# Kernel optimization log

Hardware: AMD Instinct MI355X
Metric: run time of the kernel (lower is better)

Reference implementation:

```python
import jax, jax.numpy as jnp
from jax import lax
import numpy as np

BOHR = 0.52917721067  # Angstrom per Bohr (au.BOHR)
DAMP_MUTUAL = 0.39
DAMP_FIELD = 0.7
N_ITER = 7  # fixed-point iterations for induced dipoles


def setup_inputs() -> dict:
    key = jax.random.key(0)
    N = 100000
    deg = 32
    E = N * deg
    k1, k2, k3, k4, k5, k6, k7 = jax.random.split(key, 7)
    edge_src = jax.random.randint(k1, (E,), 0, N)
    edge_dst = jax.random.randint(k2, (E,), 0, N)
    # realistic interatomic distances in [1, 6] Angstrom (avoid r ~ 0)
    distances = 1.0 + 5.0 * jax.random.uniform(k3, (E,), dtype=jnp.float32)
    u = jax.random.normal(k4, (E, 3), dtype=jnp.float32)
    u = u / jnp.linalg.norm(u, axis=-1, keepdims=True)
    vec = u * distances[:, None]  # consistent |vec| == distances
    polarisability = 0.5 + 1.5 * jax.random.uniform(k5, (N,), dtype=jnp.float32)
    charges = 0.3 * jax.random.normal(k6, (N,), dtype=jnp.float32)
    species = jax.random.randint(k7, (N,), 1, 10)
    return {
        "species": species,
        "edge_src": edge_src,
        "edge_dst": edge_dst,
        "distances": distances,
        "vec": vec,
        "polarisability": polarisability,
        "charges": charges,
    }


def reference(species, edge_src, edge_dst, distances, vec, polarisability, charges):
    N = polarisability.shape[0]
    # convert to atomic units
    rij = distances / BOHR                      # [E]
    vec_ij = vec / BOHR                         # [E,3]
    pol = polarisability.reshape(-1) / BOHR**3  # [N]

    # Thole damping: u_ij^3 = r^3 / sqrt(alpha_i * alpha_j)
    alpha_ij = pol[edge_src] * pol[edge_dst]
    uij3 = rij**3 / jnp.sqrt(alpha_ij)
    exp_m = jnp.exp(-DAMP_MUTUAL * uij3)
    l3_m = 1.0 - exp_m
    l5_m = 1.0 - (1.0 + DAMP_MUTUAL * uij3) * exp_m
    l3_f = 1.0 - jnp.exp(-DAMP_FIELD * uij3)

    inv_r3 = 1.0 / rij**3
    inv_r5 = inv_r3 / rij**2

    # permanent (charge) electric field at src atoms, Thole-damped
    e_edges = (l3_f * charges[edge_dst] * inv_r3)[:, None] * vec_ij  # [E,3]
    E0 = jax.ops.segment_sum(e_edges, edge_src, num_segments=N)      # [N,3]

    alpha = pol[:, None]  # isotropic polarisability [N,1]

    def matvec(mu):
        # Thole-damped dipole-dipole interaction tensor applied to mu: (T mu)_i
        mu_d = mu[edge_dst]                                   # [E,3]
        dot = jnp.sum(vec_ij * mu_d, axis=-1)                 # [E]
        t = (l3_m * inv_r3)[:, None] * mu_d \
            - (3.0 * l5_m * inv_r5 * dot)[:, None] * vec_ij   # [E,3]
        return jax.ops.segment_sum(t, edge_src, num_segments=N)

    # iterative induced dipoles: mu = alpha * (E0 - T mu)
    mu0 = alpha * E0

    def step(mu, _):
        return alpha * (E0 - matvec(mu)), None

    mu, _ = lax.scan(step, mu0, None, length=N_ITER)

    # per-atom polarisation energy: -1/2 mu . E0
    energy = -0.5 * jnp.sum(mu * E0, axis=-1)  # [N]
    return energy
```

## Files before the change

### kernel.cpp

```cpp
#include <hip/hip_runtime.h>
#include <hip/hip_fp16.h>


static constexpr float INV_B  = 1.0f / 0.52917721067f;
static constexpr float INV_B3 = INV_B * INV_B * INV_B;
static constexpr float DM = 0.39f;
static constexpr float DF = 0.7f;
static constexpr int   NITER = 7;
#define SCAN_B 1024
#define STAGE 4096
#define BUILD_T 512
#define MAXBUCK 512

__device__ inline unsigned packh2(float a, float b) {
    return (unsigned)__half_as_ushort(__float2half_rn(a)) |
           ((unsigned)__half_as_ushort(__float2half_rn(b)) << 16);
}
__device__ inline float unph_lo(unsigned u) {
    return __half2float(__ushort_as_half((unsigned short)(u & 0xFFFFu)));
}
__device__ inline float unph_hi(unsigned u) {
    return __half2float(__ushort_as_half((unsigned short)(u >> 16)));
}


__global__ void bhist_kernel(const int* __restrict__ esrc, int* __restrict__ h,
                             int E, int nbuck, int nblk, int chunk)
{
    __shared__ int cnt[MAXBUCK];
    int tid = threadIdx.x, blk = blockIdx.x;
    for (int b = tid; b < nbuck; b += blockDim.x) cnt[b] = 0;
    __syncthreads();
    int lo = blk * chunk, hi = min(E, lo + chunk);
    for (int i = lo + tid; i < hi; i += blockDim.x)
        atomicAdd(&cnt[esrc[i] >> 8], 1);
    __syncthreads();
    for (int b = tid; b < nbuck; b += blockDim.x)
        h[b * nblk + blk] = cnt[b];
}


__global__ void scan1_kernel(const int* __restrict__ in, int* __restrict__ excl,
                             int* __restrict__ blocksum, int n)
{
    __shared__ int sh[SCAN_B];
    int tid = threadIdx.x;
    int i = blockIdx.x * SCAN_B + tid;
    int v = (i < n) ? in[i] : 0;
    sh[tid] = v;
    __syncthreads();
    for (int off = 1; off < SCAN_B; off <<= 1) {
        int t = (tid >= off) ? sh[tid - off] : 0;
        __syncthreads();
        sh[tid] += t;
        __syncthreads();
    }
    if (i < n) excl[i] = sh[tid] - v;
    if (tid == SCAN_B - 1) blocksum[blockIdx.x] = sh[tid];
}

__global__ void scan2_kernel(int* __restrict__ blocksum, int nb)
{
    __shared__ int sh[1024];
    int tid = threadIdx.x;
    int v = (tid < nb) ? blocksum[tid] : 0;
    sh[tid] = v;
    __syncthreads();
    for (int off = 1; off < 1024; off <<= 1) {
        int t = (tid >= off) ? sh[tid - off] : 0;
        __syncthreads();
        sh[tid] += t;
        __syncthreads();
    }
    if (tid < nb) blocksum[tid] = sh[tid] - v;
}

__global__ void scan3_kernel(int* __restrict__ excl, const int* __restrict__ blocksum, int n)
{
    int i = blockIdx.x * SCAN_B + threadIdx.x;
    if (i < n) excl[i] += blocksum[blockIdx.x];
}


__global__ void bktptr_kernel(const int* __restrict__ hoff,
                              int* __restrict__ bktptr, int* __restrict__ rowptr,
                              int nbuck, int nblk, int N, int E)
{
    int b = blockIdx.x * blockDim.x + threadIdx.x;
    if (b < nbuck) bktptr[b] = hoff[b * nblk];
    if (b == nbuck) {
        bktptr[b] = E;
        if (rowptr) rowptr[N] = E;
    }
}


__global__ __launch_bounds__(BUILD_T)
void build_kernel(const int* __restrict__ esrc, const int* __restrict__ edst,
                  const float* __restrict__ dist, const float* __restrict__ vec,
                  const float* __restrict__ pol, const float* __restrict__ chg,
                  const int* __restrict__ hoff,
                  uint4* __restrict__ recs, int E, int nbuck, int nblk, int chunk)
{
    __shared__ uint4 stg[STAGE];
    __shared__ unsigned short sbuck[STAGE];
    __shared__ int wcur[MAXBUCK];
    __shared__ int shist[MAXBUCK];
    __shared__ int sbase[MAXBUCK];
    __shared__ int scur[MAXBUCK];
    __shared__ int wsum[8];
    int tid = threadIdx.x, blk = blockIdx.x;
    int lane = tid & 63, wav = tid >> 6;
    int lo = blk * chunk, hi = min(E, lo + chunk), cnt = hi - lo;

    if (tid < nbuck) wcur[tid] = hoff[tid * nblk + blk];
    __syncthreads();

    int nsb = (cnt + STAGE - 1) / STAGE;
    for (int sb = 0; sb < nsb; ++sb) {
        int s0 = sb * STAGE, s1 = min(cnt, s0 + STAGE), scnt = s1 - s0;
        if (tid < nbuck) shist[tid] = 0;
        __syncthreads();
        for (int i = s0 + tid; i < s1; i += BUILD_T)
            atomicAdd(&shist[esrc[lo + i] >> 8], 1);
        __syncthreads();
        int v = (tid < nbuck) ? shist[tid] : 0;
        int x = v;
        #pragma unroll
        for (int off = 1; off < 64; off <<= 1) {
            int t = __shfl_up(x, off);
            if (lane >= off) x += t;
        }
        if (lane == 63) wsum[wav] = x;
        __syncthreads();
        if (tid < 8) {
            int w = wsum[tid];
            #pragma unroll
            for (int off = 1; off < 8; off <<= 1) {
                int t = __shfl_up(w, off, 8);
                if (tid >= off) w += t;
            }
            wsum[tid] = w;
        }
        __syncthreads();
        int base = (wav > 0) ? wsum[wav - 1] : 0;
        if (tid < nbuck) {
            int ex = x + base - v;
            sbase[tid] = ex;
            scur[tid]  = ex;
        }
        __syncthreads();
        for (int i = s0 + tid; i < s1; i += BUILD_T) {
            int gi = lo + i;
            int s = esrc[gi], d = edst[gi];
            int b = s >> 8;
            float r  = dist[gi] * INV_B;
            float vx = vec[3*gi+0] * INV_B;
            float vy = vec[3*gi+1] * INV_B;
            float vz = vec[3*gi+2] * INV_B;
            float ps = pol[s] * INV_B3;
            float pd = pol[d] * INV_B3;
            float r2 = r * r;
            float r3 = r2 * r;
            float u  = r3 * rsqrtf(ps * pd);
            float em = __expf(-DM * u);
            float l3m = 1.0f - em;
            float l5m = 1.0f - (1.0f + DM * u) * em;
            float inv_r3 = 1.0f / r3;
            float inv_r5 = inv_r3 / r2;
            float c1 = l3m * inv_r3;
            float sw = sqrtf(3.0f * l5m * inv_r5);
            float ec = (1.0f - __expf(-DF * u)) * chg[d] * inv_r3;
            float g  = ec / sw;
            uint4 rc;
            rc.x = (unsigned)(d | ((s & 255) << 20));
            rc.y = __float_as_uint(c1);
            rc.z = packh2(sw * vx, sw * vy);
            rc.w = packh2(sw * vz, g);
            int sl = atomicAdd(&scur[b], 1);
            stg[sl]   = rc;
            sbuck[sl] = (unsigned short)b;
        }
        __syncthreads();
        for (int k = tid; k < scnt; k += BUILD_T) {
            int b = sbuck[k];
            recs[wcur[b] + (k - sbase[b])] = stg[k];
        }
        __syncthreads();
        if (tid < nbuck) wcur[tid] += shist[tid];
        __syncthreads();
    }
}


__global__ void sort_kernel(const int* __restrict__ bktptr,
                            const uint4* __restrict__ recs_raw,
                            unsigned* __restrict__ srt,
                            int* __restrict__ rowptr, const float* __restrict__ pol,
                            float4* __restrict__ E0, float4* __restrict__ mu, int N)
{
    __shared__ int hist[256];
    __shared__ int cur[256];
    __shared__ float acc[256 * 3];
    __shared__ int wsum4[4];
    int tid = threadIdx.x, b = blockIdx.x;
    int lane = tid & 63, wav = tid >> 6;
    int j0 = bktptr[b], j1 = bktptr[b + 1];
    if (tid < 256) hist[tid] = 0;
    for (int k = tid; k < 768; k += blockDim.x) acc[k] = 0.f;
    __syncthreads();
    for (int j = j0 + tid; j < j1; j += blockDim.x)
        atomicAdd(&hist[recs_raw[j].x >> 20], 1);
    __syncthreads();
    int v = (tid < 256) ? hist[tid] : 0;
    int x = v;
    #pragma unroll
    for (int off = 1; off < 64; off <<= 1) {
        int t = __shfl_up(x, off);
        if (lane >= off) x += t;
    }
    if (lane == 63 && wav < 4) wsum4[wav] = x;
    __syncthreads();
    if (tid < 4) {
        int w = wsum4[tid];
        #pragma unroll
        for (int off = 1; off < 4; off <<= 1) {
            int t = __shfl_up(w, off, 4);
            if (tid >= off) w += t;
        }
        wsum4[tid] = w;
    }
    __syncthreads();
    if (tid < 256) {
        int base = (wav > 0) ? wsum4[wav - 1] : 0;
        int beg = j0 + x + base - v;
        cur[tid] = beg;
        int row = b * 256 + tid;
        if (row < N) rowptr[row] = beg;
    }
    __syncthreads();
    for (int j = j0 + tid; j < j1; j += blockDim.x) {
        uint4 rc = recs_raw[j];
        int lr = (int)(rc.x >> 20);
        int slot = atomicAdd(&cur[lr], 1);
        float c1 = __uint_as_float(rc.y);
        float wx = unph_lo(rc.z), wy = unph_hi(rc.z);
        float wz = unph_lo(rc.w), g  = unph_hi(rc.w);
        srt[3*slot+0] = rc.x;
        srt[3*slot+1] = packh2(c1, wx);
        srt[3*slot+2] = packh2(wy, wz);
        atomicAdd(&acc[lr*3+0], g * wx);
        atomicAdd(&acc[lr*3+1], g * wy);
        atomicAdd(&acc[lr*3+2], g * wz);
    }
    __syncthreads();
    if (tid < 256) {
        int row = b * 256 + tid;
        if (row < N) {
            float ax = acc[tid*3], ay = acc[tid*3+1], az = acc[tid*3+2];
            E0[row] = make_float4(ax, ay, az, 0.f);
            float a = pol[row] * INV_B3;
            mu[row] = make_float4(a * ax, a * ay, a * az, 0.f);
        }
    }
}


__global__ void mvg_kernel(const int* __restrict__ rowptr,
                           const unsigned* __restrict__ srt, const float4* __restrict__ E0,
                           const float* __restrict__ pol,
                           const float4* __restrict__ mu_in, float4* __restrict__ mu_out,
                           float* __restrict__ energy, int N, int final_iter)
{
    int tid  = threadIdx.x;
    int lane = tid & 15;
    int row  = (blockIdx.x * blockDim.x + tid) >> 4;
    if (row >= N) return;
    int r0 = rowptr[row], r1 = rowptr[row + 1];
    float ax = 0.f, ay = 0.f, az = 0.f;
    for (int j = r0 + lane; j < r1; j += 16) {
        unsigned pk = srt[3*j+0];
        unsigned w0 = srt[3*j+1];
        unsigned w1 = srt[3*j+2];
        float4 m = mu_in[pk & 0xFFFFF];
        float c1 = unph_lo(w0);
        float wx = unph_hi(w0), wy = unph_lo(w1), wz = unph_hi(w1);
        float dot = wx * m.x + wy * m.y + wz * m.z;
        ax += c1 * m.x - dot * wx;
        ay += c1 * m.y - dot * wy;
        az += c1 * m.z - dot * wz;
    }
    for (int msk = 8; msk >= 1; msk >>= 1) {
        ax += __shfl_xor(ax, msk);
        ay += __shfl_xor(ay, msk);
        az += __shfl_xor(az, msk);
    }
    if (lane == 0) {
        float4 e0 = E0[row];
        float a = pol[row] * INV_B3;
        float mx = a * (e0.x - ax);
        float my = a * (e0.y - ay);
        float mz = a * (e0.z - az);
        mu_out[row] = make_float4(mx, my, mz, 0.f);
        if (final_iter)
            energy[row] = -0.5f * (mx * e0.x + my * e0.y + mz * e0.z);
    }
}


__global__ void e0b_kernel(const int* __restrict__ bktptr, const uint4* __restrict__ recs,
                           const float* __restrict__ pol,
                           float4* __restrict__ E0, float4* __restrict__ mu, int N)
{
    __shared__ float acc[256 * 3];
    int tid = threadIdx.x, b = blockIdx.x;
    for (int k = tid; k < 768; k += 256) acc[k] = 0.f;
    __syncthreads();
    int j0 = bktptr[b], j1 = bktptr[b + 1];
    for (int j = j0 + tid; j < j1; j += 256) {
        uint4 rc = recs[j];
        int lr = (int)(rc.x >> 20) & 255;
        float g = unph_hi(rc.w);
        atomicAdd(&acc[lr*3+0], g * unph_lo(rc.z));
        atomicAdd(&acc[lr*3+1], g * unph_hi(rc.z));
        atomicAdd(&acc[lr*3+2], g * unph_lo(rc.w));
    }
    __syncthreads();
    int r = b * 256 + tid;
    if (r < N) {
        float ax = acc[tid*3], ay = acc[tid*3+1], az = acc[tid*3+2];
        E0[r] = make_float4(ax, ay, az, 0.f);
        float a = pol[r] * INV_B3;
        mu[r] = make_float4(a * ax, a * ay, a * az, 0.f);
    }
}

__global__ void mvb_kernel(const int* __restrict__ bktptr, const uint4* __restrict__ recs,
                           const float4* __restrict__ E0, const float* __restrict__ pol,
                           const float4* __restrict__ mu_in, float4* __restrict__ mu_out,
                           float* __restrict__ energy, int N, int final_iter)
{
    __shared__ float acc[256 * 3];
    int tid = threadIdx.x, b = blockIdx.x;
    for (int k = tid; k < 768; k += 256) acc[k] = 0.f;
    __syncthreads();
    int j0 = bktptr[b], j1 = bktptr[b + 1];
    for (int j = j0 + tid; j < j1; j += 256) {
        uint4 rc = recs[j];
        float4 m = mu_in[rc.x & 0xFFFFF];
        float c1 = __uint_as_float(rc.y);
        float wx = unph_lo(rc.z), wy = unph_hi(rc.z), wz = unph_lo(rc.w);
        float dot = wx * m.x + wy * m.y + wz * m.z;
        int lr = (int)(rc.x >> 20) & 255;
        atomicAdd(&acc[lr*3+0], c1 * m.x - dot * wx);
        atomicAdd(&acc[lr*3+1], c1 * m.y - dot * wy);
        atomicAdd(&acc[lr*3+2], c1 * m.z - dot * wz);
    }
    __syncthreads();
    int r = b * 256 + tid;
    if (r < N) {
        float4 e0 = E0[r];
        float a = pol[r] * INV_B3;
        float mx = a * (e0.x - acc[tid*3+0]);
        float my = a * (e0.y - acc[tid*3+1]);
        float mz = a * (e0.z - acc[tid*3+2]);
        mu_out[r] = make_float4(mx, my, mz, 0.f);
        if (final_iter)
            energy[r] = -0.5f * (mx * e0.x + my * e0.y + mz * e0.z);
    }
}


__global__ void fb_e0_kernel(const int* esrc, const int* edst, const float* dist,
                             const float* vec, const float* pol, const float* chg,
                             float4* E0, int E)
{
    int e = blockIdx.x * blockDim.x + threadIdx.x;
    if (e >= E) return;
    int s = esrc[e], d = edst[e];
    float r  = dist[e] * INV_B;
    float vx = vec[3*e+0]*INV_B, vy = vec[3*e+1]*INV_B, vz = vec[3*e+2]*INV_B;
    float r3 = r*r*r;
    float u  = r3 * rsqrtf(pol[s]*INV_B3 * pol[d]*INV_B3);
    float ec = (1.0f - __expf(-DF*u)) * chg[d] / r3;
    atomicAdd(&E0[s].x, ec*vx); atomicAdd(&E0[s].y, ec*vy); atomicAdd(&E0[s].z, ec*vz);
}

__global__ void fb_init_kernel(const float* pol, const float4* E0, float4* mu, float4* acc, int N)
{
    int i = blockIdx.x * blockDim.x + threadIdx.x;
    if (i >= N) return;
    float a = pol[i]*INV_B3; float4 e0 = E0[i];
    mu[i]  = make_float4(a*e0.x, a*e0.y, a*e0.z, 0.f);
    acc[i] = make_float4(0.f,0.f,0.f,0.f);
}

__global__ void fb_matvec_kernel(const int* esrc, const int* edst, const float* dist,
                                 const float* vec, const float* pol,
                                 const float4* mu, float4* acc, int E)
{
    int e = blockIdx.x * blockDim.x + threadIdx.x;
    if (e >= E) return;
    int s = esrc[e], d = edst[e];
    float r  = dist[e]*INV_B;
    float vx = vec[3*e+0]*INV_B, vy = vec[3*e+1]*INV_B, vz = vec[3*e+2]*INV_B;
    float r2 = r*r, r3 = r2*r;
    float u  = r3 * rsqrtf(pol[s]*INV_B3 * pol[d]*INV_B3);
    float em = __expf(-DM*u);
    float c1 = (1.0f - em) / r3;
    float c2 = 3.0f * (1.0f - (1.0f + DM*u)*em) / (r3*r2);
    float4 m = mu[d];
    float k = c2 * (vx*m.x + vy*m.y + vz*m.z);
    atomicAdd(&acc[s].x, c1*m.x - k*vx);
    atomicAdd(&acc[s].y, c1*m.y - k*vy);
    atomicAdd(&acc[s].z, c1*m.z - k*vz);
}

__global__ void fb_update_kernel(const float* pol, const float4* E0, float4* acc,
                                 float4* mu, float* energy, int N, int final_iter)
{
    int i = blockIdx.x * blockDim.x + threadIdx.x;
    if (i >= N) return;
    float a = pol[i]*INV_B3; float4 e0 = E0[i]; float4 ac = acc[i];
    float mx = a*(e0.x-ac.x), my = a*(e0.y-ac.y), mz = a*(e0.z-ac.z);
    mu[i]  = make_float4(mx,my,mz,0.f);
    acc[i] = make_float4(0.f,0.f,0.f,0.f);
    if (final_iter) energy[i] = -0.5f*(mx*e0.x + my*e0.y + mz*e0.z);
}


static inline size_t align_up(size_t x, size_t a) { return (x + a - 1) & ~(a - 1); }

struct Layout {
    int chunk, nblk, nScan, g1;
    size_t o_h, o_hoff, o_bsum, o_bkt, o_E0, o_mua, o_mub, o_recs;
    size_t need_mid;
    size_t o_rowptr, o_srt;
    size_t need_sort;
};

static Layout make_layout(int E, int N, int nbuck, int chunk)
{
    Layout L;
    L.chunk = chunk;
    L.nblk  = (E + chunk - 1) / chunk;
    L.nScan = nbuck * L.nblk;
    L.g1    = (L.nScan + SCAN_B - 1) / SCAN_B;
    size_t off = 0;
    auto carve = [&](size_t bytes) { size_t o = off; off = align_up(off + bytes, 256); return o; };
    L.o_h      = carve((size_t)L.nScan * 4);
    L.o_hoff   = carve((size_t)L.nScan * 4);
    L.o_bsum   = carve(1024 * 4);
    L.o_bkt    = carve((size_t)(nbuck + 1) * 4);
    L.o_E0     = carve((size_t)N * 16);
    L.o_mua    = carve((size_t)N * 16);
    L.o_mub    = carve((size_t)N * 16);
    L.o_recs   = carve((size_t)E * 16);
    L.need_mid = off;
    L.o_rowptr = carve((size_t)(N + 1) * 4);
    L.o_srt    = carve((size_t)E * 12);
    L.need_sort = off;
    return L;
}

extern "C" void kernel_launch(void* const* d_in, const int* in_sizes, int n_in,
                              void* d_out, int out_size, void* d_ws, size_t ws_size,
                              hipStream_t stream)
{
    const int*   esrc = (const int*)  d_in[1];
    const int*   edst = (const int*)  d_in[2];
    const float* dist = (const float*)d_in[3];
    const float* vec  = (const float*)d_in[4];
    const float* pol  = (const float*)d_in[5];
    const float* chg  = (const float*)d_in[6];
    const int E = in_sizes[1];
    const int N = in_sizes[5];
    float* out = (float*)d_out;

    const int nbuck = (N + 255) >> 8;

    const int cand[3] = {8192, 16384, 32768};
    Layout L{}; bool ok_sort = false, ok_mid = false;
    for (int ci = 0; ci < 3; ++ci) {
        Layout t = make_layout(E, N, nbuck, cand[ci]);
        bool shp = (nbuck <= MAXBUCK) && (t.g1 <= 1024) && (nbuck >= 1) && (N < (1 << 20));
        if (shp && ws_size >= t.need_sort) { L = t; ok_sort = true; break; }
    }
    if (!ok_sort) {
        Layout t = make_layout(E, N, nbuck, 32768);
        bool shp = (nbuck <= MAXBUCK) && (t.g1 <= 1024) && (nbuck >= 1) && (N < (1 << 20));
        if (shp && ws_size >= t.need_mid) { L = t; ok_mid = true; }
    }

    char* ws = (char*)d_ws;

    if (ok_sort || ok_mid) {
        int*    h      = (int*)   (ws + L.o_h);
        int*    hoff   = (int*)   (ws + L.o_hoff);
        int*    bsum   = (int*)   (ws + L.o_bsum);
        int*    bktptr = (int*)   (ws + L.o_bkt);
        float4* E0     = (float4*)(ws + L.o_E0);
        float4* mu_a   = (float4*)(ws + L.o_mua);
        float4* mu_b   = (float4*)(ws + L.o_mub);
        uint4*  recs   = (uint4*) (ws + L.o_recs);
        int*    rowptr = ok_sort ? (int*)(ws + L.o_rowptr) : nullptr;

        bhist_kernel<<<L.nblk, BUILD_T, 0, stream>>>(esrc, h, E, nbuck, L.nblk, L.chunk);
        scan1_kernel<<<L.g1, SCAN_B, 0, stream>>>(h, hoff, bsum, L.nScan);
        scan2_kernel<<<1, 1024, 0, stream>>>(bsum, L.g1);
        scan3_kernel<<<L.g1, SCAN_B, 0, stream>>>(hoff, bsum, L.nScan);
        bktptr_kernel<<<(nbuck + 256) / 256, 256, 0, stream>>>(hoff, bktptr, rowptr,
                                                               nbuck, L.nblk, N, E);
        build_kernel<<<L.nblk, BUILD_T, 0, stream>>>(esrc, edst, dist, vec, pol, chg,
                                                     hoff, recs, E, nbuck, L.nblk, L.chunk);

        if (ok_sort) {
            unsigned* srt = (unsigned*)(ws + L.o_srt);

            sort_kernel<<<nbuck, 512, 0, stream>>>(bktptr, recs, srt, rowptr,
                                                   pol, E0, mu_a, N);

            const int NG16 = (N + 15) / 16;
            float4* min_ = mu_a; float4* mout_ = mu_b;
            for (int it = 0; it < NITER; ++it) {
                mvg_kernel<<<NG16, 256, 0, stream>>>(rowptr, srt, E0, pol,
                                                     min_, mout_, out, N, it == NITER - 1);
                float4* t = min_; min_ = mout_; mout_ = t;
            }
        } else {
            e0b_kernel<<<nbuck, 256, 0, stream>>>(bktptr, recs, pol, E0, mu_a, N);
            float4* min_ = mu_a; float4* mout_ = mu_b;
            for (int it = 0; it < NITER; ++it) {
                mvb_kernel<<<nbuck, 256, 0, stream>>>(bktptr, recs, E0, pol,
                                                      min_, mout_, out, N, it == NITER - 1);
                float4* t = min_; min_ = mout_; mout_ = t;
            }
        }
    } else {
        float4* E0  = (float4*)(ws);
        float4* mu  = (float4*)(ws + (size_t)N * 16);
        float4* acc = (float4*)(ws + (size_t)N * 32);
        const int EB = 256, NB = 256;
        const int EG = (E + EB - 1) / EB;
        const int NG = (N + NB - 1) / NB;
        hipMemsetAsync(E0, 0, (size_t)N * 16, stream);
        fb_e0_kernel<<<EG, EB, 0, stream>>>(esrc, edst, dist, vec, pol, chg, E0, E);
        fb_init_kernel<<<NG, NB, 0, stream>>>(pol, E0, mu, acc, N);
        for (int it = 0; it < NITER; ++it) {
            fb_matvec_kernel<<<EG, EB, 0, stream>>>(esrc, edst, dist, vec, pol, mu, acc, E);
            fb_update_kernel<<<NG, NB, 0, stream>>>(pol, E0, acc, mu, out, N, it == NITER - 1);
        }
    }
}
```

Measured before the change: 324.3 us.

## Replace per-block histogram scan with global bucket totals and atomic cursors

```diff
diff --git a/kernel.cpp b/kernel.cpp
--- a/kernel.cpp
+++ b/kernel.cpp
@@ -7,9 +7,9 @@
 static constexpr float DM = 0.39f;
 static constexpr float DF = 0.7f;
 static constexpr int   NITER = 7;
-#define SCAN_B 1024
 #define STAGE 4096
-#define BUILD_T 512
+#define BUILD_T 1024
+#define CHUNK 8192
 #define MAXBUCK 512
 
 __device__ inline unsigned packh2(float a, float b) {
@@ -24,8 +24,8 @@
 }
 
 
-__global__ void bhist_kernel(const int* __restrict__ esrc, int* __restrict__ h,
-                             int E, int nbuck, int nblk, int chunk)
+__global__ void bhist_kernel(const int* __restrict__ esrc, int* __restrict__ btot,
+                             int E, int nbuck, int chunk)
 {
     __shared__ int cnt[MAXBUCK];
     int tid = threadIdx.x, blk = blockIdx.x;
@@ -36,61 +36,46 @@
         atomicAdd(&cnt[esrc[i] >> 8], 1);
     __syncthreads();
     for (int b = tid; b < nbuck; b += blockDim.x)
-        h[b * nblk + blk] = cnt[b];
-}
-
-
-__global__ void scan1_kernel(const int* __restrict__ in, int* __restrict__ excl,
-                             int* __restrict__ blocksum, int n)
-{
-    __shared__ int sh[SCAN_B];
+        if (cnt[b]) atomicAdd(&btot[b], cnt[b]);
+}
+
+
+__global__ void bktptr_kernel(const int* __restrict__ btot,
+                              int* __restrict__ bktptr, int* __restrict__ gcur,
+                              int* __restrict__ rowptr,
+                              int nbuck, int N, int E)
+{
+    __shared__ int wsum[8];
     int tid = threadIdx.x;
-    int i = blockIdx.x * SCAN_B + tid;
-    int v = (i < n) ? in[i] : 0;
-    sh[tid] = v;
-    __syncthreads();
-    for (int off = 1; off < SCAN_B; off <<= 1) {
-        int t = (tid >= off) ? sh[tid - off] : 0;
-        __syncthreads();
-        sh[tid] += t;
-        __syncthreads();
-    }
-    if (i < n) excl[i] = sh[tid] - v;
-    if (tid == SCAN_B - 1) blocksum[blockIdx.x] = sh[tid];
-}
-
-__global__ void scan2_kernel(int* __restrict__ blocksum, int nb)
-{
-    __shared__ int sh[1024];
-    int tid = threadIdx.x;
-    int v = (tid < nb) ? blocksum[tid] : 0;
-    sh[tid] = v;
-    __syncthreads();
-    for (int off = 1; off < 1024; off <<= 1) {
-        int t = (tid >= off) ? sh[tid - off] : 0;
-        __syncthreads();
-        sh[tid] += t;
-        __syncthreads();
-    }
-    if (tid < nb) blocksum[tid] = sh[tid] - v;
-}
-
-__global__ void scan3_kernel(int* __restrict__ excl, const int* __restrict__ blocksum, int n)
-{
-    int i = blockIdx.x * SCAN_B + threadIdx.x;
-    if (i < n) excl[i] += blocksum[blockIdx.x];
-}
-
-
-__global__ void bktptr_kernel(const int* __restrict__ hoff,
-                              int* __restrict__ bktptr, int* __restrict__ rowptr,
-                              int nbuck, int nblk, int N, int E)
-{
-    int b = blockIdx.x * blockDim.x + threadIdx.x;
-    if (b < nbuck) bktptr[b] = hoff[b * nblk];
-    if (b == nbuck) {
-        bktptr[b] = E;
-        if (rowptr) rowptr[N] = E;
+    int lane = tid & 63, wav = tid >> 6;
+    int v = (tid < nbuck) ? btot[tid] : 0;
+    int x = v;
+    #pragma unroll
+    for (int off = 1; off < 64; off <<= 1) {
+        int t = __shfl_up(x, off);
+        if (lane >= off) x += t;
+    }
+    if (lane == 63) wsum[wav] = x;
+    __syncthreads();
+    if (tid < 8) {
+        int w = wsum[tid];
+        #pragma unroll
+        for (int off = 1; off < 8; off <<= 1) {
+            int t = __shfl_up(w, off, 8);
+            if (tid >= off) w += t;
+        }
+        wsum[tid] = w;
+    }
+    __syncthreads();
+    int base = (wav > 0) ? wsum[wav - 1] : 0;
+    if (tid < nbuck) {
+        int beg = x + base - v;
+        bktptr[tid] = beg;
+        gcur[tid]   = beg;
+    }
+    if (tid == 0) {
+        bktptr[nbuck] = E;
+        rowptr[N] = E;
     }
 }
 
@@ -99,22 +84,19 @@
 void build_kernel(const int* __restrict__ esrc, const int* __restrict__ edst,
                   const float* __restrict__ dist, const float* __restrict__ vec,
                   const float* __restrict__ pol, const float* __restrict__ chg,
-                  const int* __restrict__ hoff,
-                  uint4* __restrict__ recs, int E, int nbuck, int nblk, int chunk)
+                  int* __restrict__ gcur,
+                  uint4* __restrict__ recs, int E, int nbuck, int chunk)
 {
     __shared__ uint4 stg[STAGE];
     __shared__ unsigned short sbuck[STAGE];
-    __shared__ int wcur[MAXBUCK];
+    __shared__ int wbase[MAXBUCK];
     __shared__ int shist[MAXBUCK];
     __shared__ int sbase[MAXBUCK];
     __shared__ int scur[MAXBUCK];
-    __shared__ int wsum[8];
+    __shared__ int wsum[16];
     int tid = threadIdx.x, blk = blockIdx.x;
     int lane = tid & 63, wav = tid >> 6;
     int lo = blk * chunk, hi = min(E, lo + chunk), cnt = hi - lo;
-
-    if (tid < nbuck) wcur[tid] = hoff[tid * nblk + blk];
-    __syncthreads();
 
     int nsb = (cnt + STAGE - 1) / STAGE;
     for (int sb = 0; sb < nsb; ++sb) {
@@ -133,11 +115,11 @@
         }
         if (lane == 63) wsum[wav] = x;
         __syncthreads();
-        if (tid < 8) {
+        if (tid < 16) {
             int w = wsum[tid];
             #pragma unroll
-            for (int off = 1; off < 8; off <<= 1) {
-                int t = __shfl_up(w, off, 8);
+            for (int off = 1; off < 16; off <<= 1) {
+                int t = __shfl_up(w, off, 16);
                 if (tid >= off) w += t;
             }
             wsum[tid] = w;
@@ -148,6 +130,7 @@
             int ex = x + base - v;
             sbase[tid] = ex;
             scur[tid]  = ex;
+            wbase[tid] = v ? atomicAdd(&gcur[tid], v) : 0;
         }
         __syncthreads();
         for (int i = s0 + tid; i < s1; i += BUILD_T) {
@@ -184,20 +167,19 @@
         __syncthreads();
         for (int k = tid; k < scnt; k += BUILD_T) {
             int b = sbuck[k];
-            recs[wcur[b] + (k - sbase[b])] = stg[k];
-        }
-        __syncthreads();
-        if (tid < nbuck) wcur[tid] += shist[tid];
-        __syncthreads();
-    }
-}
-
-
-__global__ void sort_kernel(const int* __restrict__ bktptr,
-                            const uint4* __restrict__ recs_raw,
-                            unsigned* __restrict__ srt,
-                            int* __restrict__ rowptr, const float* __restrict__ pol,
-                            float4* __restrict__ E0, float4* __restrict__ mu, int N)
+            recs[wbase[b] + (k - sbase[b])] = stg[k];
+        }
+        __syncthreads();
+    }
+}
+
+
+__global__ __launch_bounds__(1024)
+void sort_kernel(const int* __restrict__ bktptr,
+                 const uint4* __restrict__ recs_raw,
+                 unsigned* __restrict__ srt,
+                 int* __restrict__ rowptr, const float* __restrict__ pol,
+                 float4* __restrict__ E0, float4* __restrict__ mu, int N)
 {
     __shared__ int hist[256];
     __shared__ int cur[256];
@@ -308,69 +290,6 @@
 }
 
 
-__global__ void e0b_kernel(const int* __restrict__ bktptr, const uint4* __restrict__ recs,
-                           const float* __restrict__ pol,
-                           float4* __restrict__ E0, float4* __restrict__ mu, int N)
-{
-    __shared__ float acc[256 * 3];
-    int tid = threadIdx.x, b = blockIdx.x;
-    for (int k = tid; k < 768; k += 256) acc[k] = 0.f;
-    __syncthreads();
-    int j0 = bktptr[b], j1 = bktptr[b + 1];
-    for (int j = j0 + tid; j < j1; j += 256) {
-        uint4 rc = recs[j];
-        int lr = (int)(rc.x >> 20) & 255;
-        float g = unph_hi(rc.w);
-        atomicAdd(&acc[lr*3+0], g * unph_lo(rc.z));
-        atomicAdd(&acc[lr*3+1], g * unph_hi(rc.z));
-        atomicAdd(&acc[lr*3+2], g * unph_lo(rc.w));
-    }
-    __syncthreads();
-    int r = b * 256 + tid;
-    if (r < N) {
-        float ax = acc[tid*3], ay = acc[tid*3+1], az = acc[tid*3+2];
-        E0[r] = make_float4(ax, ay, az, 0.f);
-        float a = pol[r] * INV_B3;
-        mu[r] = make_float4(a * ax, a * ay, a * az, 0.f);
-    }
-}
-
-__global__ void mvb_kernel(const int* __restrict__ bktptr, const uint4* __restrict__ recs,
-                           const float4* __restrict__ E0, const float* __restrict__ pol,
-                           const float4* __restrict__ mu_in, float4* __restrict__ mu_out,
-                           float* __restrict__ energy, int N, int final_iter)
-{
-    __shared__ float acc[256 * 3];
-    int tid = threadIdx.x, b = blockIdx.x;
-    for (int k = tid; k < 768; k += 256) acc[k] = 0.f;
-    __syncthreads();
-    int j0 = bktptr[b], j1 = bktptr[b + 1];
-    for (int j = j0 + tid; j < j1; j += 256) {
-        uint4 rc = recs[j];
-        float4 m = mu_in[rc.x & 0xFFFFF];
-        float c1 = __uint_as_float(rc.y);
-        float wx = unph_lo(rc.z), wy = unph_hi(rc.z), wz = unph_lo(rc.w);
-        float dot = wx * m.x + wy * m.y + wz * m.z;
-        int lr = (int)(rc.x >> 20) & 255;
-        atomicAdd(&acc[lr*3+0], c1 * m.x - dot * wx);
-        atomicAdd(&acc[lr*3+1], c1 * m.y - dot * wy);
-        atomicAdd(&acc[lr*3+2], c1 * m.z - dot * wz);
-    }
-    __syncthreads();
-    int r = b * 256 + tid;
-    if (r < N) {
-        float4 e0 = E0[r];
-        float a = pol[r] * INV_B3;
-        float mx = a * (e0.x - acc[tid*3+0]);
-        float my = a * (e0.y - acc[tid*3+1]);
-        float mz = a * (e0.z - acc[tid*3+2]);
-        mu_out[r] = make_float4(mx, my, mz, 0.f);
-        if (final_iter)
-            energy[r] = -0.5f * (mx * e0.x + my * e0.y + mz * e0.z);
-    }
-}
-
-
 __global__ void fb_e0_kernel(const int* esrc, const int* edst, const float* dist,
                              const float* vec, const float* pol, const float* chg,
                              float4* E0, int E)
@@ -431,38 +350,6 @@
 
 static inline size_t align_up(size_t x, size_t a) { return (x + a - 1) & ~(a - 1); }
 
-struct Layout {
-    int chunk, nblk, nScan, g1;
-    size_t o_h, o_hoff, o_bsum, o_bkt, o_E0, o_mua, o_mub, o_recs;
-    size_t need_mid;
-    size_t o_rowptr, o_srt;
-    size_t need_sort;
-};
-
-static Layout make_layout(int E, int N, int nbuck, int chunk)
-{
-    Layout L;
-    L.chunk = chunk;
-    L.nblk  = (E + chunk - 1) / chunk;
-    L.nScan = nbuck * L.nblk;
-    L.g1    = (L.nScan + SCAN_B - 1) / SCAN_B;
-    size_t off = 0;
-    auto carve = [&](size_t bytes) { size_t o = off; off = align_up(off + bytes, 256); return o; };
-    L.o_h      = carve((size_t)L.nScan * 4);
-    L.o_hoff   = carve((size_t)L.nScan * 4);
-    L.o_bsum   = carve(1024 * 4);
-    L.o_bkt    = carve((size_t)(nbuck + 1) * 4);
-    L.o_E0     = carve((size_t)N * 16);
-    L.o_mua    = carve((size_t)N * 16);
-    L.o_mub    = carve((size_t)N * 16);
-    L.o_recs   = carve((size_t)E * 16);
-    L.need_mid = off;
-    L.o_rowptr = carve((size_t)(N + 1) * 4);
-    L.o_srt    = carve((size_t)E * 12);
-    L.need_sort = off;
-    return L;
-}
-
 extern "C" void kernel_launch(void* const* d_in, const int* in_sizes, int n_in,
                               void* d_out, int out_size, void* d_ws, size_t ws_size,
                               hipStream_t stream)
@@ -478,63 +365,49 @@
     float* out = (float*)d_out;
 
     const int nbuck = (N + 255) >> 8;
-
-    const int cand[3] = {8192, 16384, 32768};
-    Layout L{}; bool ok_sort = false, ok_mid = false;
-    for (int ci = 0; ci < 3; ++ci) {
-        Layout t = make_layout(E, N, nbuck, cand[ci]);
-        bool shp = (nbuck <= MAXBUCK) && (t.g1 <= 1024) && (nbuck >= 1) && (N < (1 << 20));
-        if (shp && ws_size >= t.need_sort) { L = t; ok_sort = true; break; }
-    }
-    if (!ok_sort) {
-        Layout t = make_layout(E, N, nbuck, 32768);
-        bool shp = (nbuck <= MAXBUCK) && (t.g1 <= 1024) && (nbuck >= 1) && (N < (1 << 20));
-        if (shp && ws_size >= t.need_mid) { L = t; ok_mid = true; }
-    }
+    const int nblk  = (E + CHUNK - 1) / CHUNK;
 
     char* ws = (char*)d_ws;
-
-    if (ok_sort || ok_mid) {
-        int*    h      = (int*)   (ws + L.o_h);
-        int*    hoff   = (int*)   (ws + L.o_hoff);
-        int*    bsum   = (int*)   (ws + L.o_bsum);
-        int*    bktptr = (int*)   (ws + L.o_bkt);
-        float4* E0     = (float4*)(ws + L.o_E0);
-        float4* mu_a   = (float4*)(ws + L.o_mua);
-        float4* mu_b   = (float4*)(ws + L.o_mub);
-        uint4*  recs   = (uint4*) (ws + L.o_recs);
-        int*    rowptr = ok_sort ? (int*)(ws + L.o_rowptr) : nullptr;
-
-        bhist_kernel<<<L.nblk, BUILD_T, 0, stream>>>(esrc, h, E, nbuck, L.nblk, L.chunk);
-        scan1_kernel<<<L.g1, SCAN_B, 0, stream>>>(h, hoff, bsum, L.nScan);
-        scan2_kernel<<<1, 1024, 0, stream>>>(bsum, L.g1);
-        scan3_kernel<<<L.g1, SCAN_B, 0, stream>>>(hoff, bsum, L.nScan);
-        bktptr_kernel<<<(nbuck + 256) / 256, 256, 0, stream>>>(hoff, bktptr, rowptr,
-                                                               nbuck, L.nblk, N, E);
-        build_kernel<<<L.nblk, BUILD_T, 0, stream>>>(esrc, edst, dist, vec, pol, chg,
-                                                     hoff, recs, E, nbuck, L.nblk, L.chunk);
-
-        if (ok_sort) {
-            unsigned* srt = (unsigned*)(ws + L.o_srt);
-
-            sort_kernel<<<nbuck, 512, 0, stream>>>(bktptr, recs, srt, rowptr,
-                                                   pol, E0, mu_a, N);
-
-            const int NG16 = (N + 15) / 16;
-            float4* min_ = mu_a; float4* mout_ = mu_b;
-            for (int it = 0; it < NITER; ++it) {
-                mvg_kernel<<<NG16, 256, 0, stream>>>(rowptr, srt, E0, pol,
-                                                     min_, mout_, out, N, it == NITER - 1);
-                float4* t = min_; min_ = mout_; mout_ = t;
-            }
-        } else {
-            e0b_kernel<<<nbuck, 256, 0, stream>>>(bktptr, recs, pol, E0, mu_a, N);
-            float4* min_ = mu_a; float4* mout_ = mu_b;
-            for (int it = 0; it < NITER; ++it) {
-                mvb_kernel<<<nbuck, 256, 0, stream>>>(bktptr, recs, E0, pol,
-                                                      min_, mout_, out, N, it == NITER - 1);
-                float4* t = min_; min_ = mout_; mout_ = t;
-            }
+    size_t off = 0;
+    auto carve = [&](size_t bytes) { size_t o = off; off = align_up(off + bytes, 256); return o; };
+    size_t o_bkt    = carve((size_t)(nbuck + 1) * 4);
+    size_t o_btot   = carve((size_t)nbuck * 4);
+    size_t o_gcur   = carve((size_t)nbuck * 4);
+    size_t o_E0     = carve((size_t)N * 16);
+    size_t o_mua    = carve((size_t)N * 16);
+    size_t o_mub    = carve((size_t)N * 16);
+    size_t o_rowptr = carve((size_t)(N + 1) * 4);
+    size_t o_recs   = carve((size_t)E * 16);
+    size_t o_srt    = carve((size_t)E * 12);
+    size_t need = off;
+
+    bool ok = (ws_size >= need) && (nbuck <= MAXBUCK) && (nbuck >= 1) && (N < (1 << 20));
+
+    if (ok) {
+        int*      bktptr = (int*)     (ws + o_bkt);
+        int*      btot   = (int*)     (ws + o_btot);
+        int*      gcur   = (int*)     (ws + o_gcur);
+        float4*   E0     = (float4*)  (ws + o_E0);
+        float4*   mu_a   = (float4*)  (ws + o_mua);
+        float4*   mu_b   = (float4*)  (ws + o_mub);
+        int*      rowptr = (int*)     (ws + o_rowptr);
+        uint4*    recs   = (uint4*)   (ws + o_recs);
+        unsigned* srt    = (unsigned*)(ws + o_srt);
+
+        hipMemsetAsync(btot, 0, (size_t)nbuck * 4, stream);
+        bhist_kernel<<<nblk, BUILD_T, 0, stream>>>(esrc, btot, E, nbuck, CHUNK);
+        bktptr_kernel<<<1, 512, 0, stream>>>(btot, bktptr, gcur, rowptr, nbuck, N, E);
+        build_kernel<<<nblk, BUILD_T, 0, stream>>>(esrc, edst, dist, vec, pol, chg,
+                                                   gcur, recs, E, nbuck, CHUNK);
+        sort_kernel<<<nbuck, 1024, 0, stream>>>(bktptr, recs, srt, rowptr,
+                                                pol, E0, mu_a, N);
+
+        const int NG16 = (N + 15) / 16;
+        float4* min_ = mu_a; float4* mout_ = mu_b;
+        for (int it = 0; it < NITER; ++it) {
+            mvg_kernel<<<NG16, 256, 0, stream>>>(rowptr, srt, E0, pol,
+                                                 min_, mout_, out, N, it == NITER - 1);
+            float4* t = min_; min_ = mout_; mout_ = t;
         }
     } else {
         float4* E0  = (float4*)(ws);
```

Result: slower. 332.6 us (+2.6%).
